# Kernel tuning notes

Measured on AMD Instinct MI355X. Metric: run time of the kernel, lower is better.

The kernel has to match this reference:

```python
import jax, jax.numpy as jnp
import numpy as np

N, E = 50000, 800000
D_IN, D_HID, D_OUT = 128, 256, 128


def setup_inputs() -> dict:
    key = jax.random.key(0)
    k = jax.random.split(key, 7)
    x = jax.random.normal(k[0], (N, D_IN), dtype=jnp.float32)
    edge_src = jax.random.randint(k[1], (E,), 0, N, dtype=jnp.int32)
    edge_dst = jax.random.randint(k[2], (E,), 0, N, dtype=jnp.int32)
    s1 = 1.0 / np.sqrt(2 * D_IN)
    s2 = 1.0 / np.sqrt(2 * D_HID)
    W1 = jax.random.uniform(k[3], (2 * D_IN, D_HID), jnp.float32, -s1, s1)
    b1 = jax.random.uniform(k[4], (D_HID,), jnp.float32, -s1, s1)
    W2 = jax.random.uniform(k[5], (2 * D_HID, D_OUT), jnp.float32, -s2, s2)
    b2 = jax.random.uniform(k[6], (D_OUT,), jnp.float32, -s2, s2)
    return {"x": x, "edge_src": edge_src, "edge_dst": edge_dst,
            "W1": W1, "b1": b1, "W2": W2, "b2": b2}


def _sage_layer(h, edge_src, edge_dst, W, b, inv_deg):
    # mean-pool neighbor features: gather [E, D] then segment-sum to [N, D]
    msgs = h[edge_src]
    agg = jax.ops.segment_sum(msgs, edge_dst, num_segments=h.shape[0]) * inv_deg
    y = jnp.concatenate([h, agg], axis=1)  # [N, 2D]
    return y @ W + b


def reference(x, edge_src, edge_dst, W1, b1, W2, b2):
    n = x.shape[0]
    deg = jax.ops.segment_sum(jnp.ones_like(edge_dst, dtype=x.dtype), edge_dst,
                              num_segments=n)
    inv_deg = (1.0 / jnp.maximum(deg, 1.0))[:, None]  # isolated nodes -> zeros
    h = _sage_layer(x, edge_src, edge_dst, W1, b1, inv_deg)
    h = jax.nn.relu(h)
    # dropout is identity in eval mode
    h = _sage_layer(h, edge_src, edge_dst, W2, b2, inv_deg)
    return jax.nn.log_softmax(h, axis=1)
```

## Files before the change

### kernel.cpp

```cpp
#include <hip/hip_runtime.h>
#include <cstdint>
#include <cstddef>

typedef __attribute__((ext_vector_type(8))) short bf16x8;
typedef __attribute__((ext_vector_type(4))) float f32x4;
typedef __attribute__((ext_vector_type(2))) float f32x2;

__device__ inline short bf16_rne(float f) {
  unsigned u = __builtin_bit_cast(unsigned, f);
  u += 0x7fff + ((u >> 16) & 1);
  return (short)(u >> 16);
}

__device__ inline float bf16lo(unsigned v) { return __builtin_bit_cast(float, v << 16); }
__device__ inline float bf16hi(unsigned v) { return __builtin_bit_cast(float, v & 0xffff0000u); }

__device__ inline unsigned pack2(float a, float b) {
  return ((unsigned)(unsigned short)bf16_rne(a)) | (((unsigned)(unsigned short)bf16_rne(b)) << 16);
}


__global__ __launch_bounds__(256) void prep_kernel(const float* __restrict__ W1,
                                                   const float* __restrict__ W2,
                                                   const float* __restrict__ b2,
                                                   const float* __restrict__ x,
                                                   short* __restrict__ B1p,
                                                   short* __restrict__ B2p,
                                                   float* __restrict__ bias2,
                                                   unsigned* __restrict__ A1u,
                                                   unsigned* __restrict__ xf8, int nquads,
                                                   int* __restrict__ counters, int NB) {
  int b = blockIdx.x;
  int tid = threadIdx.x;
  int nqb = (nquads + 255) >> 8;
  if (b < 512) {
    int mode = b >> 8;
    int idx = (b & 255) * 256 + tid;
    int j = idx & 7;
    int L = (idx >> 3) & 63;
    int nt = (idx >> 9) & 15;
    int kb = idx >> 13;
    int k = kb * 32 + (L >> 4) * 8 + j;
    int n = nt * 16 + (L & 15);
    if (mode == 0) {
      B1p[idx] = bf16_rne(W1[(size_t)k * 256 + n]);
    } else {
      float v = (n < 128) ? W2[(size_t)k * 128 + n] : W2[(size_t)(256 + k) * 128 + (n - 128)];
      B2p[idx] = bf16_rne(v);
    }
  } else if (b == 512) {
    bias2[tid] = (tid < 128) ? b2[tid] : 0.0f;
  } else if (b < 513 + nqb) {
    int idx = (b - 513) * 256 + tid;
    if (idx < nquads) {
      int n = idx >> 5, q = idx & 31;
      float4 v = ((const float4*)x)[idx];
      ((uint2*)A1u)[(size_t)n * 64 + q] = make_uint2(pack2(v.x, v.y), pack2(v.z, v.w));
      int pk = __builtin_amdgcn_cvt_pk_fp8_f32(v.x, v.y, 0, false);
      pk = __builtin_amdgcn_cvt_pk_fp8_f32(v.z, v.w, pk, true);
      xf8[(size_t)n * 32 + q] = (unsigned)pk;
    }
  } else {
    for (int t = tid; t < NB; t += 256) counters[t] = 0;
  }
}

__global__ __launch_bounds__(256) void bucket_scatter(const int* __restrict__ src,
                                                      const int* __restrict__ dst, int E, int EPB,
                                                      int* __restrict__ counters, int NB,
                                                      int SLACK, unsigned* __restrict__ bedge) {
  __shared__ int h[512];
  __shared__ int base[512];
  int tid = threadIdx.x;
  for (int t = tid; t < NB; t += 256) h[t] = 0;
  __syncthreads();
  int start = blockIdx.x * EPB, end = min(E, start + EPB);
  for (int i = start + tid; i < end; i += 256) atomicAdd(&h[((unsigned)dst[i]) >> 7], 1);
  __syncthreads();
  for (int t = tid; t < NB; t += 256) {
    int c = h[t];
    base[t] = (c > 0) ? atomicAdd(&counters[t], c) : 0;
    h[t] = 0;
  }
  __syncthreads();
  for (int i = start + tid; i < end; i += 256) {
    unsigned d = (unsigned)dst[i];
    unsigned bk = d >> 7;
    int p = base[bk] + atomicAdd(&h[bk], 1);
    bedge[(size_t)bk * SLACK + p] = ((d & 127u) << 24) | (unsigned)src[i];
  }
}

__global__ __launch_bounds__(256) void build_csr(const unsigned* __restrict__ bedge,
                                                 const int* __restrict__ counters,
                                                 int NB, int SLACK, int N,
                                                 int* __restrict__ offsets,
                                                 int* __restrict__ oend,
                                                 float* __restrict__ inv_deg,
                                                 int* __restrict__ ssrc) {
  __shared__ int buf[128];
  int b = blockIdx.x, tid = threadIdx.x;
  int cntE = counters[b];
  int rb = b * SLACK;
  if (tid < 128) buf[tid] = 0;
  __syncthreads();
  for (int i = tid; i < cntE; i += 256) atomicAdd(&buf[bedge[(size_t)rb + i] >> 24], 1);
  __syncthreads();
  int cnt = (tid < 128) ? buf[tid] : 0;
  #pragma unroll
  for (int off = 1; off < 128; off <<= 1) {
    int t = (tid >= off && tid < 128) ? buf[tid - off] : 0;
    __syncthreads();
    if (tid < 128) buf[tid] += t;
    __syncthreads();
  }
  if (tid < 128) {
    int excl_l = buf[tid] - cnt;
    int node = (b << 7) + tid;
    if (node < N) {
      offsets[node] = rb + excl_l;
      oend[node]    = rb + excl_l + cnt;
      inv_deg[node] = 1.0f / fmaxf((float)cnt, 1.0f);
    }
    buf[tid] = rb + excl_l;
  }
  __syncthreads();
  for (int i = tid; i < cntE; i += 256) {
    unsigned e2 = bedge[(size_t)rb + i];
    int p = atomicAdd(&buf[e2 >> 24], 1);
    ssrc[p] = (int)(e2 & 0xFFFFFFu);
  }
}

#define CVT8(U, A0, A1, A2, A3, A4, A5, A6, A7)                                        \
  {                                                                                    \
    f32x2 p_, q_;                                                                      \
    p_ = __builtin_amdgcn_cvt_pk_f32_fp8((U).x, false);                                \
    q_ = __builtin_amdgcn_cvt_pk_f32_fp8((U).x, true);                                 \
    A0 += p_[0]; A1 += p_[1]; A2 += q_[0]; A3 += q_[1];                                \
    p_ = __builtin_amdgcn_cvt_pk_f32_fp8((U).y, false);                                \
    q_ = __builtin_amdgcn_cvt_pk_f32_fp8((U).y, true);                                 \
    A4 += p_[0]; A5 += p_[1]; A6 += q_[0]; A7 += q_[1];                                \
  }

__global__ __launch_bounds__(256) void agg1_kernel(const uint2* __restrict__ X8,
                                                   const int* __restrict__ offsets,
                                                   const int* __restrict__ oend,
                                                   const int* __restrict__ ssrc,
                                                   const float* __restrict__ inv_deg,
                                                   uint4* __restrict__ A1q, int N) {
  int node = blockIdx.x * 4 + (threadIdx.x >> 6);
  if (node >= N) return;
  int lane = threadIdx.x & 63;
  int g = lane >> 4;
  int l = lane & 15;
  int s = offsets[node], e = oend[node];
  float a0=0.f,a1=0.f,a2=0.f,a3=0.f,a4=0.f,a5=0.f,a6=0.f,a7=0.f;
  int i = s;
  for (; i + 16 <= e; i += 16) {
    int sA = ssrc[i + g], sB = ssrc[i + 4 + g];
    int sC = ssrc[i + 8 + g], sD = ssrc[i + 12 + g];
    uint2 u = X8[((size_t)(unsigned)sA << 4) + l];
    uint2 v = X8[((size_t)(unsigned)sB << 4) + l];
    uint2 w = X8[((size_t)(unsigned)sC << 4) + l];
    uint2 z = X8[((size_t)(unsigned)sD << 4) + l];
    CVT8(u, a0,a1,a2,a3,a4,a5,a6,a7);
    CVT8(v, a0,a1,a2,a3,a4,a5,a6,a7);
    CVT8(w, a0,a1,a2,a3,a4,a5,a6,a7);
    CVT8(z, a0,a1,a2,a3,a4,a5,a6,a7);
  }
  for (; i < e; i += 4) {
    if (g < e - i) {
      uint2 u = X8[((size_t)(unsigned)ssrc[i + g] << 4) + l];
      CVT8(u, a0,a1,a2,a3,a4,a5,a6,a7);
    }
  }
  a0 += __shfl_xor(a0,16,64); a0 += __shfl_xor(a0,32,64);
  a1 += __shfl_xor(a1,16,64); a1 += __shfl_xor(a1,32,64);
  a2 += __shfl_xor(a2,16,64); a2 += __shfl_xor(a2,32,64);
  a3 += __shfl_xor(a3,16,64); a3 += __shfl_xor(a3,32,64);
  a4 += __shfl_xor(a4,16,64); a4 += __shfl_xor(a4,32,64);
  a5 += __shfl_xor(a5,16,64); a5 += __shfl_xor(a5,32,64);
  a6 += __shfl_xor(a6,16,64); a6 += __shfl_xor(a6,32,64);
  a7 += __shfl_xor(a7,16,64); a7 += __shfl_xor(a7,32,64);
  if (g == 0) {
    float id = inv_deg[node];
    A1q[((size_t)node << 5) + 16 + l] =
        make_uint4(pack2(a0 * id, a1 * id), pack2(a2 * id, a3 * id),
                   pack2(a4 * id, a5 * id), pack2(a6 * id, a7 * id));
  }
}

__global__ __launch_bounds__(256, 2) void gemm_mfma(const short* __restrict__ A,
                                                    const short* __restrict__ Bp,
                                                    const float* __restrict__ bias,
                                                    void* __restrict__ out0,
                                                    void* __restrict__ out1,
                                                    int S, int mode) {
  int tid = threadIdx.x;
  int w = tid >> 6;
  int lane = tid & 63;

  bf16x8 breg[8][4];
  #pragma unroll
  for (int kb = 0; kb < 8; ++kb)
    #pragma unroll
    for (int j = 0; j < 4; ++j)
      breg[kb][j] = *(const bf16x8*)(Bp + ((size_t)((kb * 16 + w * 4 + j) * 64 + lane)) * 8);

  float bj[4];
  #pragma unroll
  for (int j = 0; j < 4; ++j) bj[j] = bias[w * 64 + j * 16 + (lane & 15)];

  int rowInFrag = lane & 15;
  int kseg = (lane >> 4) * 8;

  for (int s = blockIdx.x; s < S; s += gridDim.x) {
    int row0 = s * 16;
    const short* Arow = A + (size_t)(row0 + rowInFrag) * 256 + kseg;
    bf16x8 afr[8];
    #pragma unroll
    for (int kb = 0; kb < 8; ++kb) afr[kb] = *(const bf16x8*)(Arow + kb * 32);

    f32x4 acc[4];
    #pragma unroll
    for (int j = 0; j < 4; ++j) acc[j] = (f32x4)(0.0f);
    #pragma unroll
    for (int kb = 0; kb < 8; ++kb)
      #pragma unroll
      for (int j = 0; j < 4; ++j)
        acc[j] = __builtin_amdgcn_mfma_f32_16x16x32_bf16(afr[kb], breg[kb][j], acc[j], 0, 0, 0);

    int crow0 = row0 + (lane >> 4) * 4;
    int ccol = lane & 15;
    #pragma unroll
    for (int j = 0; j < 4; ++j) {
      int col = w * 64 + j * 16 + ccol;
      #pragma unroll
      for (int r = 0; r < 4; ++r) {
        float v = acc[j][r] + bj[j];
        int row = crow0 + r;
        if (mode == 0) {
          ((short*)out0)[(size_t)row * 256 + col] = bf16_rne(fmaxf(v, 0.0f));
        } else if (w < 2) {
          ((short*)out0)[(size_t)row * 128 + col] = bf16_rne(v);
        } else {
          int pk = __builtin_amdgcn_cvt_pk_fp8_f32(v, v, 0, false);
          ((unsigned char*)out1)[(size_t)row * 128 + (col - 128)] = (unsigned char)(pk & 0xff);
        }
      }
    }
  }
}

__global__ __launch_bounds__(256) void final_kernel(const uint4* __restrict__ utopq,
                                                    const uint2* __restrict__ T2,
                                                    const int* __restrict__ offsets,
                                                    const int* __restrict__ oend,
                                                    const int* __restrict__ ssrc,
                                                    const float* __restrict__ inv_deg,
                                                    float4* __restrict__ out4, int N) {
  int node = blockIdx.x * 4 + (threadIdx.x >> 6);
  if (node >= N) return;
  int lane = threadIdx.x & 63;
  int g = lane >> 4;
  int l = lane & 15;
  int s = offsets[node], e = oend[node];
  float a0=0.f,a1=0.f,a2=0.f,a3=0.f,a4=0.f,a5=0.f,a6=0.f,a7=0.f;
  int i = s;
  for (; i + 16 <= e; i += 16) {
    int sA = ssrc[i + g], sB = ssrc[i + 4 + g];
    int sC = ssrc[i + 8 + g], sD = ssrc[i + 12 + g];
    uint2 u = T2[((size_t)(unsigned)sA << 4) + l];
    uint2 v = T2[((size_t)(unsigned)sB << 4) + l];
    uint2 w = T2[((size_t)(unsigned)sC << 4) + l];
    uint2 z = T2[((size_t)(unsigned)sD << 4) + l];
    CVT8(u, a0,a1,a2,a3,a4,a5,a6,a7);
    CVT8(v, a0,a1,a2,a3,a4,a5,a6,a7);
    CVT8(w, a0,a1,a2,a3,a4,a5,a6,a7);
    CVT8(z, a0,a1,a2,a3,a4,a5,a6,a7);
  }
  for (; i < e; i += 4) {
    if (g < e - i) {
      uint2 u = T2[((size_t)(unsigned)ssrc[i + g] << 4) + l];
      CVT8(u, a0,a1,a2,a3,a4,a5,a6,a7);
    }
  }
  a0 += __shfl_xor(a0,16,64); a0 += __shfl_xor(a0,32,64);
  a1 += __shfl_xor(a1,16,64); a1 += __shfl_xor(a1,32,64);
  a2 += __shfl_xor(a2,16,64); a2 += __shfl_xor(a2,32,64);
  a3 += __shfl_xor(a3,16,64); a3 += __shfl_xor(a3,32,64);
  a4 += __shfl_xor(a4,16,64); a4 += __shfl_xor(a4,32,64);
  a5 += __shfl_xor(a5,16,64); a5 += __shfl_xor(a5,32,64);
  a6 += __shfl_xor(a6,16,64); a6 += __shfl_xor(a6,32,64);
  a7 += __shfl_xor(a7,16,64); a7 += __shfl_xor(a7,32,64);
  if (g == 0) {
    float id = inv_deg[node];
    uint4 U = utopq[((size_t)node << 4) + l];
    float v0 = bf16lo(U.x) + a0 * id;
    float v1 = bf16hi(U.x) + a1 * id;
    float v2 = bf16lo(U.y) + a2 * id;
    float v3 = bf16hi(U.y) + a3 * id;
    float v4 = bf16lo(U.z) + a4 * id;
    float v5 = bf16hi(U.z) + a5 * id;
    float v6 = bf16lo(U.w) + a6 * id;
    float v7 = bf16hi(U.w) + a7 * id;
    float m = fmaxf(fmaxf(fmaxf(v0, v1), fmaxf(v2, v3)), fmaxf(fmaxf(v4, v5), fmaxf(v6, v7)));
    #pragma unroll
    for (int off = 1; off < 16; off <<= 1) m = fmaxf(m, __shfl_xor(m, off, 16));
    float su = expf(v0 - m) + expf(v1 - m) + expf(v2 - m) + expf(v3 - m) +
               expf(v4 - m) + expf(v5 - m) + expf(v6 - m) + expf(v7 - m);
    #pragma unroll
    for (int off = 1; off < 16; off <<= 1) su += __shfl_xor(su, off, 16);
    float ls = m + logf(su);
    out4[((size_t)node << 5) + l * 2]     = make_float4(v0 - ls, v1 - ls, v2 - ls, v3 - ls);
    out4[((size_t)node << 5) + l * 2 + 1] = make_float4(v4 - ls, v5 - ls, v6 - ls, v7 - ls);
  }
}

extern "C" void kernel_launch(void* const* d_in, const int* in_sizes, int n_in,
                              void* d_out, int out_size, void* d_ws, size_t ws_size,
                              hipStream_t stream) {
  const float* x        = (const float*)d_in[0];
  const int*   edge_src = (const int*)d_in[1];
  const int*   edge_dst = (const int*)d_in[2];
  const float* W1       = (const float*)d_in[3];
  const float* b1       = (const float*)d_in[4];
  const float* W2       = (const float*)d_in[5];
  const float* b2       = (const float*)d_in[6];
  float* out = (float*)d_out;

  const int D_IN = 128;
  const int N = in_sizes[0] / D_IN;
  const int E = in_sizes[1];
  const int M_pad = ((N + 127) / 128) * 128;

  const int SB = 512;
  const int EPB = (E + SB - 1) / SB;
  const int NB = (N + 127) >> 7;
  const int SLACK = 3072;

  char* ws = (char*)d_ws;
  size_t p = 0;
  auto take = [&](size_t bytes) -> size_t {
    size_t r = p;
    p += (bytes + 255) & ~(size_t)255;
    return r;
  };
  size_t cnt_off   = take((size_t)NB * 4);
  size_t bedge_off = take((size_t)NB * SLACK * 4);
  size_t offs_off  = take((size_t)N * 4);
  size_t oend_off  = take((size_t)N * 4);
  size_t inv_off   = take((size_t)N * 4);
  size_t ssrc_off  = take((size_t)NB * SLACK * 4);
  size_t A1_off    = take((size_t)M_pad * 256 * 2);
  size_t xf8_off   = take((size_t)M_pad * 128);
  size_t h_off     = take((size_t)M_pad * 256 * 2);
  size_t B1p_off   = take((size_t)256 * 256 * 2);
  size_t B2p_off   = take((size_t)256 * 256 * 2);
  size_t bias2_off = take((size_t)256 * 4);
  size_t utop_off  = take((size_t)M_pad * 128 * 2);
  size_t t2_off    = take((size_t)M_pad * 128);
  (void)ws_size;

  int*   counters = (int*)(ws + cnt_off);
  unsigned* bedge = (unsigned*)(ws + bedge_off);
  int*   offsets  = (int*)(ws + offs_off);
  int*   oendp    = (int*)(ws + oend_off);
  float* inv_deg  = (float*)(ws + inv_off);
  int*   ssrc     = (int*)(ws + ssrc_off);
  unsigned* A1u   = (unsigned*)(ws + A1_off);
  unsigned* xf8   = (unsigned*)(ws + xf8_off);
  short* h        = (short*)(ws + h_off);
  short* B1p      = (short*)(ws + B1p_off);
  short* B2p      = (short*)(ws + B2p_off);
  float* bias2    = (float*)(ws + bias2_off);
  short* utop     = (short*)(ws + utop_off);
  unsigned char* t2f8 = (unsigned char*)(ws + t2_off);

  {
    int nquads = N * 32;
    int grid = 513 + (nquads + 255) / 256 + 1;
    prep_kernel<<<grid, 256, 0, stream>>>(W1, W2, b2, x, B1p, B2p, bias2, A1u, xf8, nquads,
                                          counters, NB);
  }
  bucket_scatter<<<SB, 256, 0, stream>>>(edge_src, edge_dst, E, EPB, counters, NB, SLACK, bedge);
  build_csr<<<NB, 256, 0, stream>>>(bedge, counters, NB, SLACK, N, offsets, oendp, inv_deg, ssrc);

  agg1_kernel<<<(N + 3) / 4, 256, 0, stream>>>((const uint2*)xf8, offsets, oendp, ssrc, inv_deg,
                                               (uint4*)A1u, N);
  {
    int S = M_pad / 16;
    gemm_mfma<<<1024, 256, 0, stream>>>((const short*)A1u, B1p, b1, h, nullptr, S, 0);
    gemm_mfma<<<1024, 256, 0, stream>>>(h, B2p, bias2, utop, t2f8, S, 1);
  }
  final_kernel<<<(N + 3) / 4, 256, 0, stream>>>((const uint4*)utop, (const uint2*)t2f8,
                                                offsets, oendp, ssrc, inv_deg, (float4*)out, N);
}
```

Measured before the change: 222.3 us.

## Fuse both dense GEMMs into one producer/consumer kernel via LDS

```diff
diff --git a/kernel.cpp b/kernel.cpp
--- a/kernel.cpp
+++ b/kernel.cpp
@@ -191,15 +191,25 @@
   }
 }
 
-__global__ __launch_bounds__(256, 2) void gemm_mfma(const short* __restrict__ A,
-                                                    const short* __restrict__ Bp,
-                                                    const float* __restrict__ bias,
-                                                    void* __restrict__ out0,
-                                                    void* __restrict__ out1,
-                                                    int S, int mode) {
+__global__ __launch_bounds__(512, 2) void gemm_fused(const short* __restrict__ A,
+                                                     const short* __restrict__ B1,
+                                                     const short* __restrict__ B2,
+                                                     const float* __restrict__ bias1,
+                                                     const float* __restrict__ bias2,
+                                                     short* __restrict__ utop,
+                                                     unsigned char* __restrict__ t2,
+                                                     int S) {
+  __shared__ char hls[2 * 16 * 512];
   int tid = threadIdx.x;
-  int w = tid >> 6;
+  int wv = tid >> 6;
   int lane = tid & 63;
+  int role = wv >> 2;
+  int w = wv & 3;
+  int rowf = lane & 15;
+  int g = lane >> 4;
+
+  const short* Bp = role ? B2 : B1;
+  const float* bias = role ? bias2 : bias1;
 
   bf16x8 breg[8][4];
   #pragma unroll
@@ -208,48 +218,88 @@
     for (int j = 0; j < 4; ++j)
       breg[kb][j] = *(const bf16x8*)(Bp + ((size_t)((kb * 16 + w * 4 + j) * 64 + lane)) * 8);
 
-  float bj[4];
+  f32x4 bj[4];
   #pragma unroll
-  for (int j = 0; j < 4; ++j) bj[j] = bias[w * 64 + j * 16 + (lane & 15)];
-
-  int rowInFrag = lane & 15;
-  int kseg = (lane >> 4) * 8;
-
-  for (int s = blockIdx.x; s < S; s += gridDim.x) {
-    int row0 = s * 16;
-    const short* Arow = A + (size_t)(row0 + rowInFrag) * 256 + kseg;
-    bf16x8 afr[8];
-    #pragma unroll
-    for (int kb = 0; kb < 8; ++kb) afr[kb] = *(const bf16x8*)(Arow + kb * 32);
-
-    f32x4 acc[4];
-    #pragma unroll
-    for (int j = 0; j < 4; ++j) acc[j] = (f32x4)(0.0f);
-    #pragma unroll
-    for (int kb = 0; kb < 8; ++kb)
-      #pragma unroll
-      for (int j = 0; j < 4; ++j)
-        acc[j] = __builtin_amdgcn_mfma_f32_16x16x32_bf16(afr[kb], breg[kb][j], acc[j], 0, 0, 0);
-
-    int crow0 = row0 + (lane >> 4) * 4;
-    int ccol = lane & 15;
-    #pragma unroll
-    for (int j = 0; j < 4; ++j) {
-      int col = w * 64 + j * 16 + ccol;
-      #pragma unroll
-      for (int r = 0; r < 4; ++r) {
-        float v = acc[j][r] + bj[j];
-        int row = crow0 + r;
-        if (mode == 0) {
-          ((short*)out0)[(size_t)row * 256 + col] = bf16_rne(fmaxf(v, 0.0f));
-        } else if (w < 2) {
-          ((short*)out0)[(size_t)row * 128 + col] = bf16_rne(v);
-        } else {
-          int pk = __builtin_amdgcn_cvt_pk_fp8_f32(v, v, 0, false);
-          ((unsigned char*)out1)[(size_t)row * 128 + (col - 128)] = (unsigned char)(pk & 0xff);
+  for (int j = 0; j < 4; ++j)
+    bj[j] = *(const f32x4*)(bias + w * 64 + j * 16 + g * 4);
+
+  for (int i = 0;; ++i) {
+    int sP = blockIdx.x + i * gridDim.x;
+    int sC = blockIdx.x + (i - 1) * gridDim.x;
+    bool anyP = sP < S;
+    bool anyC = (i > 0) && (sC < S);
+    if (!anyP && !anyC) break;
+
+    if (role == 0) {
+      if (anyP) {
+        int row0 = sP * 16;
+        const short* Arow = A + (size_t)(row0 + rowf) * 256 + g * 8;
+        bf16x8 afr[8];
+        #pragma unroll
+        for (int kb = 0; kb < 8; ++kb) afr[kb] = *(const bf16x8*)(Arow + kb * 32);
+        f32x4 acc[4];
+        #pragma unroll
+        for (int j = 0; j < 4; ++j) acc[j] = (f32x4)(0.0f);
+        __builtin_amdgcn_s_setprio(1);
+        #pragma unroll
+        for (int kb = 0; kb < 8; ++kb)
+          #pragma unroll
+          for (int j = 0; j < 4; ++j)
+            acc[j] = __builtin_amdgcn_mfma_f32_16x16x32_bf16(breg[kb][j], afr[kb], acc[j], 0, 0, 0);
+        __builtin_amdgcn_s_setprio(0);
+        int buf = (i & 1) * 8192;
+        #pragma unroll
+        for (int j = 0; j < 4; ++j) {
+          float v0 = fmaxf(acc[j][0] + bj[j][0], 0.0f);
+          float v1 = fmaxf(acc[j][1] + bj[j][1], 0.0f);
+          float v2 = fmaxf(acc[j][2] + bj[j][2], 0.0f);
+          float v3 = fmaxf(acc[j][3] + bj[j][3], 0.0f);
+          int c0 = w * 64 + j * 16 + g * 4;
+          int chunk = c0 >> 3;
+          int swz = chunk ^ rowf ^ ((chunk & 1) << 4);
+          *(uint2*)(hls + buf + rowf * 512 + swz * 16 + ((c0 & 4) << 1)) =
+              make_uint2(pack2(v0, v1), pack2(v2, v3));
         }
       }
-    }
+    } else {
+      if (anyC) {
+        int buf = ((i - 1) & 1) * 8192;
+        bf16x8 afr[8];
+        #pragma unroll
+        for (int kb = 0; kb < 8; ++kb) {
+          int chunk = kb * 4 + g;
+          int swz = chunk ^ rowf ^ ((chunk & 1) << 4);
+          afr[kb] = *(const bf16x8*)(hls + buf + rowf * 512 + swz * 16);
+        }
+        f32x4 acc[4];
+        #pragma unroll
+        for (int j = 0; j < 4; ++j) acc[j] = (f32x4)(0.0f);
+        __builtin_amdgcn_s_setprio(1);
+        #pragma unroll
+        for (int kb = 0; kb < 8; ++kb)
+          #pragma unroll
+          for (int j = 0; j < 4; ++j)
+            acc[j] = __builtin_amdgcn_mfma_f32_16x16x32_bf16(breg[kb][j], afr[kb], acc[j], 0, 0, 0);
+        __builtin_amdgcn_s_setprio(0);
+        int row = sC * 16 + rowf;
+        #pragma unroll
+        for (int j = 0; j < 4; ++j) {
+          float v0 = acc[j][0] + bj[j][0];
+          float v1 = acc[j][1] + bj[j][1];
+          float v2 = acc[j][2] + bj[j][2];
+          float v3 = acc[j][3] + bj[j][3];
+          int c0 = w * 64 + j * 16 + g * 4;
+          if (w < 2) {
+            *(uint2*)(utop + (size_t)row * 128 + c0) = make_uint2(pack2(v0, v1), pack2(v2, v3));
+          } else {
+            int pk = __builtin_amdgcn_cvt_pk_fp8_f32(v0, v1, 0, false);
+            pk = __builtin_amdgcn_cvt_pk_fp8_f32(v2, v3, pk, true);
+            *(unsigned*)(t2 + (size_t)row * 128 + (c0 - 128)) = (unsigned)pk;
+          }
+        }
+      }
+    }
+    __syncthreads();
   }
 }
 
@@ -355,7 +405,6 @@
   size_t ssrc_off  = take((size_t)NB * SLACK * 4);
   size_t A1_off    = take((size_t)M_pad * 256 * 2);
   size_t xf8_off   = take((size_t)M_pad * 128);
-  size_t h_off     = take((size_t)M_pad * 256 * 2);
   size_t B1p_off   = take((size_t)256 * 256 * 2);
   size_t B2p_off   = take((size_t)256 * 256 * 2);
   size_t bias2_off = take((size_t)256 * 4);
@@ -371,7 +420,6 @@
   int*   ssrc     = (int*)(ws + ssrc_off);
   unsigned* A1u   = (unsigned*)(ws + A1_off);
   unsigned* xf8   = (unsigned*)(ws + xf8_off);
-  short* h        = (short*)(ws + h_off);
   short* B1p      = (short*)(ws + B1p_off);
   short* B2p      = (short*)(ws + B2p_off);
   float* bias2    = (float*)(ws + bias2_off);
@@ -391,8 +439,7 @@
                                                (uint4*)A1u, N);
   {
     int S = M_pad / 16;
-    gemm_mfma<<<1024, 256, 0, stream>>>((const short*)A1u, B1p, b1, h, nullptr, S, 0);
-    gemm_mfma<<<1024, 256, 0, stream>>>(h, B2p, bias2, utop, t2f8, S, 1);
+    gemm_fused<<<256, 512, 0, stream>>>((const short*)A1u, B1p, B2p, b1, bias2, utop, t2f8, S);
   }
   final_kernel<<<(N + 3) / 4, 256, 0, stream>>>((const uint4*)utop, (const uint2*)t2f8,
                                                 offsets, oendp, ssrc, inv_deg, (float4*)out, N);
```

Result: faster. 206.6 us (-7.1%).
